# Kernel optimization log

Hardware: AMD Instinct MI355X
Metric: run time of the kernel (lower is better)

The kernel has to match this reference:

```python
import jax, jax.numpy as jnp
import numpy as np

N = 1_000_000
F = 128
B = 4096


def setup_inputs() -> dict:
    key = jax.random.key(0)
    ks = jax.random.split(key, 10)
    x = jax.random.normal(ks[0], (N, F), dtype=jnp.float32)
    E = jax.random.normal(ks[1], (B,), dtype=jnp.float32)
    batch_seg = jnp.sort(jax.random.randint(ks[2], (N,), 0, B)).astype(jnp.int64)
    # params
    Wq = jax.random.normal(ks[3], (F, F), dtype=jnp.float32) / np.sqrt(F)
    bq = jnp.zeros((F,), dtype=jnp.float32)
    Wk = jax.random.normal(ks[4], (F, 2), dtype=jnp.float32)
    Wv = jax.random.normal(ks[5], (F, 2), dtype=jnp.float32)
    # residual MLP (num_residual=1, bias=False)
    W1 = jax.random.normal(ks[6], (F, F), dtype=jnp.float32) / np.sqrt(F)
    W2 = jax.random.normal(ks[7], (F, F), dtype=jnp.float32) / np.sqrt(F)
    return {"x": x, "E": E, "num_batch": B, "batch_seg": batch_seg,
            "Wq": Wq, "bq": bq, "Wk": Wk, "Wv": Wv, "W1": W1, "W2": W2}


def reference(x, E, num_batch, batch_seg, Wq, bq, Wk, Wv, W1, W2):
    eps = 1e-8
    q = x @ Wq.T + bq                                   # [N, F]
    e = jax.nn.relu(jnp.stack([E, -E], axis=-1))        # [B, 2]
    enorm = jnp.maximum(e, jnp.ones_like(e))
    k = ((e / enorm) @ Wk.T)[batch_seg]                 # [N, F] gather
    v = (e @ Wv.T)[batch_seg]                           # [N, F] gather
    dot = jnp.sum(k * q, axis=-1) / jnp.sqrt(jnp.float32(F))  # [N]
    a = jax.nn.softplus(dot)
    anorm = jax.ops.segment_sum(a, batch_seg, num_segments=num_batch)  # [B]
    attn = (a / (anorm[batch_seg] + eps))[:, None]      # [N, 1]
    h = attn * v                                        # [N, F]
    # ResidualMLP, 1 block, bias=False: h = h + W2(silu(W1(silu(h))))
    res = jax.nn.silu(jax.nn.silu(h) @ W1.T) @ W2.T
    return h + res
```

## Files before the change

kernel.cpp:

```cpp
#include <hip/hip_runtime.h>

constexpr int kN = 1000000;
constexpr int kF = 128;
constexpr int kB = 4096;

using short8 = __attribute__((ext_vector_type(8))) short;
using f32x4 = __attribute__((ext_vector_type(4))) float;

__device__ __forceinline__ unsigned short to_bf16(float f) {
  unsigned int u = __builtin_bit_cast(unsigned int, f);
  u += 0x7fffu + ((u >> 16) & 1u);
  return (unsigned short)(u >> 16);
}

__device__ __forceinline__ float silu_f(float z) {
  return z / (1.f + __expf(-z));
}

__global__ __launch_bounds__(128) void k_precompute(
    const float* __restrict__ E, const float* __restrict__ Wq,
    const float* __restrict__ bq, const float* __restrict__ Wk,
    const float* __restrict__ Wv, float* __restrict__ u,
    float* __restrict__ v, float* __restrict__ cb,
    float* __restrict__ anorm) {
  __shared__ float ksh[kF];
  const int b = blockIdx.x;
  const int f = threadIdx.x;
  const float Eb = E[b];
  const float e0 = fmaxf(Eb, 0.f);
  const float e1 = fmaxf(-Eb, 0.f);
  const float en0 = e0 / fmaxf(e0, 1.f);
  const float en1 = e1 / fmaxf(e1, 1.f);
  const float kf = Wk[2 * f + 0] * en0 + Wk[2 * f + 1] * en1;
  const float vf = Wv[2 * f + 0] * e0 + Wv[2 * f + 1] * e1;
  v[b * kF + f] = vf;
  ksh[f] = kf;
  __syncthreads();
  float uj = 0.f;
#pragma unroll 8
  for (int ff = 0; ff < kF; ++ff) uj = fmaf(Wq[ff * kF + f], ksh[ff], uj);
  u[b * kF + f] = uj;
  if (f == 0) {
    float c = 0.f;
    for (int ff = 0; ff < kF; ++ff) c = fmaf(bq[ff], ksh[ff], c);
    cb[b] = c;
    anorm[b] = 0.f;
  }
}

__global__ __launch_bounds__(256) void k_pass1(
    const float* __restrict__ x, const int* __restrict__ seg,
    const float* __restrict__ u, const float* __restrict__ cb,
    float* __restrict__ a, float* __restrict__ anorm) {
  const int lane = threadIdx.x & 63;
  const int g = lane >> 4;
  const int c = lane & 15;
  const int wave = (int)((blockIdx.x * blockDim.x + threadIdx.x) >> 6);
  const int nw = (int)((gridDim.x * blockDim.x) >> 6);
  const int cpw = (((kN + nw - 1) / nw) + 3) & ~3;
  const int r0 = wave * cpw;
  const int r1 = min(kN, r0 + cpw);
  int bacc = -1;
  float ssum = 0.f;
  for (int rb = r0; rb < r1; rb += 4) {
    const int row = rb + g;
    const int b = seg[row];
    const float* xr = x + (size_t)row * kF + c * 8;
    const float* ur = u + (size_t)b * kF + c * 8;
    const float4 xa = *reinterpret_cast<const float4*>(xr);
    const float4 xb = *reinterpret_cast<const float4*>(xr + 4);
    const float4 ua = *reinterpret_cast<const float4*>(ur);
    const float4 ub = *reinterpret_cast<const float4*>(ur + 4);
    float p = xa.x * ua.x;
    p = fmaf(xa.y, ua.y, p);
    p = fmaf(xa.z, ua.z, p);
    p = fmaf(xa.w, ua.w, p);
    p = fmaf(xb.x, ub.x, p);
    p = fmaf(xb.y, ub.y, p);
    p = fmaf(xb.z, ub.z, p);
    p = fmaf(xb.w, ub.w, p);
#pragma unroll
    for (int o = 1; o < 16; o <<= 1) p += __shfl_xor(p, o);
    const float dot = (p + cb[b]) * 0.08838834764831845f;
    const float av = fmaxf(dot, 0.f) + __logf(1.f + __expf(-fabsf(dot)));
    if (c == 0) a[row] = av;
#pragma unroll
    for (int gg = 0; gg < 4; ++gg) {
      const float avg = __shfl(av, 16 * gg);
      const int bg = __shfl(b, 16 * gg);
      if (lane == 0) {
        if (bg != bacc) {
          if (bacc >= 0) atomicAdd(anorm + bacc, ssum);
          bacc = bg;
          ssum = 0.f;
        }
        ssum += avg;
      }
    }
  }
  if (lane == 0 && bacc >= 0) atomicAdd(anorm + bacc, ssum);
}

constexpr int kWaves = 12;
constexpr int kStg = 40;

__global__ __launch_bounds__(768) void k_pass2(
    const int* __restrict__ seg, const float* __restrict__ a,
    const float* __restrict__ anorm, const float* __restrict__ v,
    const float* __restrict__ W1, const float* __restrict__ W2,
    float* __restrict__ out) {
  __shared__ __align__(16) unsigned short Wf[2 * 16384];
  __shared__ __align__(16) unsigned short stg[kWaves][32 * kStg];
  const int tid = threadIdx.x;
  for (int idx = tid; idx < 2 * 16384; idx += 768) {
    const int mtx = idx >> 14;
    const int e = idx & 16383;
    const int i = e & 7;
    const int l = (e >> 3) & 63;
    const int kb = (e >> 9) & 3;
    const int nb = (e >> 11) & 7;
    const int row = nb * 16 + (l & 15);
    const int col = kb * 32 + ((l >> 4) & 3) * 8 + i;
    const float w = (mtx ? W2 : W1)[row * kF + col];
    Wf[idx] = to_bf16(w);
  }
  __syncthreads();

  const int wid = tid >> 6;
  const int lane = tid & 63;
  const int c = lane & 15;
  const int g = lane >> 4;
  unsigned short* __restrict__ st = stg[wid];

  const int gw = blockIdx.x * kWaves + wid;
  const int nw = gridDim.x * kWaves;
  const int niter = kN / 32;

  for (int it = gw; it < niter; it += nw) {
    const int rbase = it * 32;
    int bb[2];
    float attn[2];
    short8 t1[2][4];
#pragma unroll
    for (int mt = 0; mt < 2; ++mt) {
      const int row = rbase + mt * 16 + c;
      const int b = seg[row];
      bb[mt] = b;
      const float at = a[row] / (anorm[b] + 1e-8f);
      attn[mt] = at;
      const float* vrow = v + (size_t)b * kF;
#pragma unroll
      for (int kb = 0; kb < 4; ++kb) {
        const int k0 = kb * 32 + g * 8;
        const float4 va = *reinterpret_cast<const float4*>(vrow + k0);
        const float4 vb = *reinterpret_cast<const float4*>(vrow + k0 + 4);
        short8 fr;
        fr[0] = (short)to_bf16(silu_f(at * va.x));
        fr[1] = (short)to_bf16(silu_f(at * va.y));
        fr[2] = (short)to_bf16(silu_f(at * va.z));
        fr[3] = (short)to_bf16(silu_f(at * va.w));
        fr[4] = (short)to_bf16(silu_f(at * vb.x));
        fr[5] = (short)to_bf16(silu_f(at * vb.y));
        fr[6] = (short)to_bf16(silu_f(at * vb.z));
        fr[7] = (short)to_bf16(silu_f(at * vb.w));
        t1[mt][kb] = fr;
      }
    }

    f32x4 acc2[2][8];
#pragma unroll
    for (int mt = 0; mt < 2; ++mt)
#pragma unroll
      for (int jb = 0; jb < 8; ++jb) acc2[mt][jb] = (f32x4){0.f, 0.f, 0.f, 0.f};

#pragma unroll
    for (int p = 0; p < 4; ++p) {
      f32x4 z[2][2];
#pragma unroll
      for (int mt = 0; mt < 2; ++mt)
#pragma unroll
        for (int nb = 0; nb < 2; ++nb) z[mt][nb] = (f32x4){0.f, 0.f, 0.f, 0.f};
#pragma unroll
      for (int kb = 0; kb < 4; ++kb) {
        const short8 w0 = *reinterpret_cast<const short8*>(
            &Wf[(((2 * p + 0) * 4 + kb) * 64 + lane) * 8]);
        const short8 w1 = *reinterpret_cast<const short8*>(
            &Wf[(((2 * p + 1) * 4 + kb) * 64 + lane) * 8]);
        z[0][0] = __builtin_amdgcn_mfma_f32_16x16x32_bf16(t1[0][kb], w0,
                                                          z[0][0], 0, 0, 0);
        z[0][1] = __builtin_amdgcn_mfma_f32_16x16x32_bf16(t1[0][kb], w1,
                                                          z[0][1], 0, 0, 0);
        z[1][0] = __builtin_amdgcn_mfma_f32_16x16x32_bf16(t1[1][kb], w0,
                                                          z[1][0], 0, 0, 0);
        z[1][1] = __builtin_amdgcn_mfma_f32_16x16x32_bf16(t1[1][kb], w1,
                                                          z[1][1], 0, 0, 0);
      }
#pragma unroll
      for (int mt = 0; mt < 2; ++mt)
#pragma unroll
        for (int nb = 0; nb < 2; ++nb)
#pragma unroll
          for (int r = 0; r < 4; ++r) {
            const int srow = mt * 16 + g * 4 + r;
            const int scol = nb * 16 + c;
            st[srow * kStg + scol] = to_bf16(silu_f(z[mt][nb][r]));
          }
      short8 t2f[2];
#pragma unroll
      for (int mt = 0; mt < 2; ++mt)
        t2f[mt] = *reinterpret_cast<const short8*>(
            &st[(mt * 16 + c) * kStg + g * 8]);
#pragma unroll
      for (int jb = 0; jb < 8; ++jb) {
        const short8 w2f = *reinterpret_cast<const short8*>(
            &Wf[16384 + ((jb * 4 + p) * 64 + lane) * 8]);
        acc2[0][jb] = __builtin_amdgcn_mfma_f32_16x16x32_bf16(t2f[0], w2f,
                                                              acc2[0][jb], 0, 0, 0);
        acc2[1][jb] = __builtin_amdgcn_mfma_f32_16x16x32_bf16(t2f[1], w2f,
                                                              acc2[1][jb], 0, 0, 0);
      }
    }

#pragma unroll
    for (int mt = 0; mt < 2; ++mt) {
      int b4[4];
      float at4[4];
#pragma unroll
      for (int r = 0; r < 4; ++r) {
        b4[r] = __shfl(bb[mt], g * 4 + r);
        at4[r] = __shfl(attn[mt], g * 4 + r);
      }
#pragma unroll
      for (int jb = 0; jb < 8; ++jb) {
#pragma unroll
        for (int r = 0; r < 4; ++r) {
          const int row = rbase + mt * 16 + g * 4 + r;
          const int col = jb * 16 + c;
          const float vv = v[(size_t)b4[r] * kF + col];
          out[(size_t)row * kF + col] = fmaf(at4[r], vv, acc2[mt][jb][r]);
        }
      }
    }
  }
}

extern "C" void kernel_launch(void* const* d_in, const int* in_sizes, int n_in,
                              void* d_out, int out_size, void* d_ws,
                              size_t ws_size, hipStream_t stream) {
  const float* x = (const float*)d_in[0];
  const float* E = (const float*)d_in[1];
  const int* seg = (const int*)d_in[3];
  const float* Wq = (const float*)d_in[4];
  const float* bq = (const float*)d_in[5];
  const float* Wk = (const float*)d_in[6];
  const float* Wv = (const float*)d_in[7];
  const float* W1 = (const float*)d_in[8];
  const float* W2 = (const float*)d_in[9];
  float* out = (float*)d_out;

  float* u = (float*)d_ws;
  float* v = u + (size_t)kB * kF;
  float* cb = v + (size_t)kB * kF;
  float* anorm = cb + kB;
  float* a = anorm + kB;

  k_precompute<<<kB, kF, 0, stream>>>(E, Wq, bq, Wk, Wv, u, v, cb, anorm);
  k_pass1<<<2048, 256, 0, stream>>>(x, seg, u, cb, a, anorm);
  k_pass2<<<256, 768, 0, stream>>>(seg, a, anorm, v, W1, W2, out);
}
```

Before: 414.0 us.

## Permute MFMA weight layout to vectorize output stores and staging writes

The W1/W2 fragments in shared memory are stored with permuted output rows, so each lane's accumulator columns become contiguous. This lets the epilogue write two float4 per row instead of eight scalar stores, and lets the silu staging write packed 32-bit pairs. Pass1 is also reworked to handle eight rows per iteration, with each 16-lane group accumulating its own segment partials, which removes the serialized lane-0 shuffle loop. The trade-off is more atomics in pass1, and correctness now depends on the permutation matching the MFMA output mapping.

```diff
diff --git a/kernel.cpp b/kernel.cpp
--- a/kernel.cpp
+++ b/kernel.cpp
@@ -57,48 +57,53 @@
   const int c = lane & 15;
   const int wave = (int)((blockIdx.x * blockDim.x + threadIdx.x) >> 6);
   const int nw = (int)((gridDim.x * blockDim.x) >> 6);
-  const int cpw = (((kN + nw - 1) / nw) + 3) & ~3;
+  const int cpw = (((kN + nw - 1) / nw) + 7) & ~7;
   const int r0 = wave * cpw;
   const int r1 = min(kN, r0 + cpw);
   int bacc = -1;
   float ssum = 0.f;
-  for (int rb = r0; rb < r1; rb += 4) {
-    const int row = rb + g;
-    const int b = seg[row];
-    const float* xr = x + (size_t)row * kF + c * 8;
-    const float* ur = u + (size_t)b * kF + c * 8;
-    const float4 xa = *reinterpret_cast<const float4*>(xr);
-    const float4 xb = *reinterpret_cast<const float4*>(xr + 4);
-    const float4 ua = *reinterpret_cast<const float4*>(ur);
-    const float4 ub = *reinterpret_cast<const float4*>(ur + 4);
-    float p = xa.x * ua.x;
-    p = fmaf(xa.y, ua.y, p);
-    p = fmaf(xa.z, ua.z, p);
-    p = fmaf(xa.w, ua.w, p);
-    p = fmaf(xb.x, ub.x, p);
-    p = fmaf(xb.y, ub.y, p);
-    p = fmaf(xb.z, ub.z, p);
-    p = fmaf(xb.w, ub.w, p);
-#pragma unroll
-    for (int o = 1; o < 16; o <<= 1) p += __shfl_xor(p, o);
-    const float dot = (p + cb[b]) * 0.08838834764831845f;
-    const float av = fmaxf(dot, 0.f) + __logf(1.f + __expf(-fabsf(dot)));
-    if (c == 0) a[row] = av;
-#pragma unroll
-    for (int gg = 0; gg < 4; ++gg) {
-      const float avg = __shfl(av, 16 * gg);
-      const int bg = __shfl(b, 16 * gg);
-      if (lane == 0) {
-        if (bg != bacc) {
+  for (int rb = r0; rb < r1; rb += 8) {
+    float av2[2];
+    int b2[2];
+#pragma unroll
+    for (int q = 0; q < 2; ++q) {
+      const int row = rb + 4 * q + g;
+      const int b = seg[row];
+      const float* xr = x + (size_t)row * kF + c * 8;
+      const float* ur = u + (size_t)b * kF + c * 8;
+      const float4 xa = *reinterpret_cast<const float4*>(xr);
+      const float4 xb = *reinterpret_cast<const float4*>(xr + 4);
+      const float4 ua = *reinterpret_cast<const float4*>(ur);
+      const float4 ub = *reinterpret_cast<const float4*>(ur + 4);
+      float p = xa.x * ua.x;
+      p = fmaf(xa.y, ua.y, p);
+      p = fmaf(xa.z, ua.z, p);
+      p = fmaf(xa.w, ua.w, p);
+      p = fmaf(xb.x, ub.x, p);
+      p = fmaf(xb.y, ub.y, p);
+      p = fmaf(xb.z, ub.z, p);
+      p = fmaf(xb.w, ub.w, p);
+#pragma unroll
+      for (int o = 1; o < 16; o <<= 1) p += __shfl_xor(p, o);
+      const float dot = (p + cb[b]) * 0.08838834764831845f;
+      const float av = fmaxf(dot, 0.f) + __logf(1.f + __expf(-fabsf(dot)));
+      av2[q] = av;
+      b2[q] = b;
+      if (c == 0) a[row] = av;
+    }
+    if (c == 0) {
+#pragma unroll
+      for (int q = 0; q < 2; ++q) {
+        if (b2[q] != bacc) {
           if (bacc >= 0) atomicAdd(anorm + bacc, ssum);
-          bacc = bg;
+          bacc = b2[q];
           ssum = 0.f;
         }
-        ssum += avg;
-      }
-    }
-  }
-  if (lane == 0 && bacc >= 0) atomicAdd(anorm + bacc, ssum);
+        ssum += av2[q];
+      }
+    }
+  }
+  if (c == 0 && bacc >= 0) atomicAdd(anorm + bacc, ssum);
 }
 
 constexpr int kWaves = 12;
@@ -119,8 +124,10 @@
     const int l = (e >> 3) & 63;
     const int kb = (e >> 9) & 3;
     const int nb = (e >> 11) & 7;
-    const int row = nb * 16 + (l & 15);
+    const int cc = l & 15;
     const int col = kb * 32 + ((l >> 4) & 3) * 8 + i;
+    const int row = mtx ? (cc * 8 + nb)
+                        : ((nb >> 1) * 32 + 2 * cc + (nb & 1));
     const float w = (mtx ? W2 : W1)[row * kF + col];
     Wf[idx] = to_bf16(w);
   }
@@ -198,13 +205,12 @@
 #pragma unroll
       for (int mt = 0; mt < 2; ++mt)
 #pragma unroll
-        for (int nb = 0; nb < 2; ++nb)
-#pragma unroll
-          for (int r = 0; r < 4; ++r) {
-            const int srow = mt * 16 + g * 4 + r;
-            const int scol = nb * 16 + c;
-            st[srow * kStg + scol] = to_bf16(silu_f(z[mt][nb][r]));
-          }
+        for (int r = 0; r < 4; ++r) {
+          const unsigned int lo = to_bf16(silu_f(z[mt][0][r]));
+          const unsigned int hi = to_bf16(silu_f(z[mt][1][r]));
+          *reinterpret_cast<unsigned int*>(
+              &st[(mt * 16 + g * 4 + r) * kStg + 2 * c]) = lo | (hi << 16);
+        }
       short8 t2f[2];
 #pragma unroll
       for (int mt = 0; mt < 2; ++mt)
@@ -223,22 +229,27 @@
 
 #pragma unroll
     for (int mt = 0; mt < 2; ++mt) {
-      int b4[4];
-      float at4[4];
 #pragma unroll
       for (int r = 0; r < 4; ++r) {
-        b4[r] = __shfl(bb[mt], g * 4 + r);
-        at4[r] = __shfl(attn[mt], g * 4 + r);
-      }
-#pragma unroll
-      for (int jb = 0; jb < 8; ++jb) {
-#pragma unroll
-        for (int r = 0; r < 4; ++r) {
-          const int row = rbase + mt * 16 + g * 4 + r;
-          const int col = jb * 16 + c;
-          const float vv = v[(size_t)b4[r] * kF + col];
-          out[(size_t)row * kF + col] = fmaf(at4[r], vv, acc2[mt][jb][r]);
-        }
+        const int src = g * 4 + r;
+        const int b4 = __shfl(bb[mt], src);
+        const float at4 = __shfl(attn[mt], src);
+        const float* vr = v + (size_t)b4 * kF + c * 8;
+        const float4 vlo = *reinterpret_cast<const float4*>(vr);
+        const float4 vhi = *reinterpret_cast<const float4*>(vr + 4);
+        const size_t row = (size_t)(rbase + mt * 16 + g * 4 + r);
+        float* orow = out + row * kF + c * 8;
+        float4 olo, ohi;
+        olo.x = fmaf(at4, vlo.x, acc2[mt][0][r]);
+        olo.y = fmaf(at4, vlo.y, acc2[mt][1][r]);
+        olo.z = fmaf(at4, vlo.z, acc2[mt][2][r]);
+        olo.w = fmaf(at4, vlo.w, acc2[mt][3][r]);
+        ohi.x = fmaf(at4, vhi.x, acc2[mt][4][r]);
+        ohi.y = fmaf(at4, vhi.y, acc2[mt][5][r]);
+        ohi.z = fmaf(at4, vhi.z, acc2[mt][6][r]);
+        ohi.w = fmaf(at4, vhi.w, acc2[mt][7][r]);
+        *reinterpret_cast<float4*>(orow) = olo;
+        *reinterpret_cast<float4*>(orow + 4) = ohi;
       }
     }
   }
```

Result: slower. 725.7 us (+75.3%).
